# Performance work log

Hardware: AMD Instinct MI355X
Metric: run time of the kernel (lower is better)

The kernel has to match this reference:

```python
import jax, jax.numpy as jnp
import numpy as np

jax.config.update("jax_enable_x64", True)

N_QUBITS = 21
N_LAYERS = 2
N_PARAMS = (N_LAYERS + 1) * N_QUBITS  # 63

# CNOT in |ctrl,tgt> basis, reshaped to (c_out, t_out, c_in, t_in)
_CNOT = jnp.array([[1, 0, 0, 0],
                   [0, 1, 0, 0],
                   [0, 0, 0, 1],
                   [0, 0, 1, 0]], dtype=jnp.complex128).reshape(2, 2, 2, 2)


def _ry(theta):
    # RY(theta) = [[cos(t/2), -sin(t/2)], [sin(t/2), cos(t/2)]]
    c = jnp.cos(theta * 0.5).astype(jnp.complex128)
    s = jnp.sin(theta * 0.5).astype(jnp.complex128)
    return jnp.stack([jnp.stack([c, -s]), jnp.stack([s, c])])


def _apply_1q(state, gate, q):
    # Contract 2x2 gate into qubit axis q of the (2,)*n state tensor.
    state = jnp.tensordot(gate, state, axes=((1,), (q,)))
    return jnp.moveaxis(state, 0, q)


def _apply_cnot(state, q):
    # CNOT with control q, target q+1 (qubit 0 = most-significant axis).
    state = jnp.tensordot(_CNOT, state, axes=((2, 3), (q, q + 1)))
    return jnp.moveaxis(state, (0, 1), (q, q + 1))


def setup_inputs() -> dict:
    key = jax.random.key(0)
    params = jax.random.uniform(key, (N_PARAMS,), dtype=jnp.float32) * (2.0 * np.pi)
    return {"params": params}


def reference(params):
    p = params.astype(jnp.float64)
    # |0...0> as a (2,)*n tensor
    state = jnp.zeros((2,) * N_QUBITS, dtype=jnp.complex128)
    state = state.at[(0,) * N_QUBITS].set(1.0 + 0.0j)
    idx = 0
    for _ in range(N_LAYERS):
        for q in range(N_QUBITS):
            state = _apply_1q(state, _ry(p[idx]), q)
            idx += 1
        for q in range(N_QUBITS - 1):
            state = _apply_cnot(state, q)
    for q in range(N_QUBITS):
        state = _apply_1q(state, _ry(p[idx]), q)
        idx += 1
    state = state.reshape(-1)  # (2**N_QUBITS,)
    return state / jnp.linalg.norm(state)
```

## Files before the change

kernel.cpp:

```cpp
#include <hip/hip_runtime.h>


#define NQ 21
#define NSTATE (1 << NQ)
#define SW(t) ((t) + ((t) >> 5))

typedef float f32x4 __attribute__((ext_vector_type(4)));

__device__ __forceinline__ float sel(const float* cs, const float* sn, int i,
                                     int bit) {
  return bit ? sn[i] : cs[i];
}

template <int BIT, int N>
__device__ __forceinline__ void ry_bf(float (&v)[N], float c, float s) {
#pragma unroll
  for (int m = 0; m < N; ++m)
    if ((m & (1 << BIT)) == 0) {
      float a = v[m], b = v[m | (1 << BIT)];
      v[m] = c * a - s * b;
      v[m | (1 << BIT)] = s * a + c * b;
    }
}

template <int CBIT, int TBIT, int N>
__device__ __forceinline__ void cnot_rr(float (&v)[N]) {
#pragma unroll
  for (int m = 0; m < N; ++m)
    if ((m & (1 << CBIT)) && !(m & (1 << TBIT))) {
      float t = v[m];
      v[m] = v[m | (1 << TBIT)];
      v[m | (1 << TBIT)] = t;
    }
}

template <int TBIT, int N>
__device__ __forceinline__ void cswap_bf(float (&v)[N], bool cond) {
#pragma unroll
  for (int m = 0; m < N; ++m)
    if ((m & (1 << TBIT)) == 0) {
      float a = v[m], b = v[m | (1 << TBIT)];
      v[m] = cond ? b : a;
      v[m | (1 << TBIT)] = cond ? a : b;
    }
}

template <int MASK, int N>
__device__ __forceinline__ void ry_shfl(float (&u)[N], float c, float s,
                                        int lane) {
  const float ss = (lane & MASK) ? s : -s;
#pragma unroll
  for (int e = 0; e < N; ++e) {
    float w = __shfl_xor(u[e], MASK);
    u[e] = c * u[e] + ss * w;
  }
}

template <int CMASK, int TMASK, int N>
__device__ __forceinline__ void cnot_shfl(float (&u)[N], int lane) {
  const bool ctrl = (lane & CMASK) != 0;
#pragma unroll
  for (int e = 0; e < N; ++e) {
    float w = __shfl_xor(u[e], TMASK);
    u[e] = ctrl ? w : u[e];
  }
}

__global__ __launch_bounds__(512) void fused(const float* __restrict__ p,
                                             float* __restrict__ out,
                                             int outmode) {
  __shared__ float cs[63], sn[63];
  __shared__ float ex[8448];
  const int tid = threadIdx.x;
  const int bid = blockIdx.x;
  if (tid < 63) {
    float h = 0.5f * p[tid];
    cs[tid] = cosf(h);
    sn[tid] = sinf(h);
  }
  __syncthreads();

  const int lane = tid & 63;
  float u[16];
  {
    const int zh = (lane & 31) << 4;
    const int c = lane >> 5;
#pragma unroll
    for (int e = 0; e < 16; ++e) {
      const int z = zh | e;
      const int gz = z ^ (z >> 1);
      float F = sel(cs, sn, 0, (z >> 8) & 1);
#pragma unroll
      for (int j = 0; j < 8; ++j) F *= sel(cs, sn, 8 - j, (gz >> j) & 1);
      u[e] = ((z & 1) == c) ? F : 0.0f;
    }
  }
  ry_shfl<16>(u, cs[21], sn[21], lane);
  ry_shfl<8>(u, cs[22], sn[22], lane);
  ry_shfl<4>(u, cs[23], sn[23], lane);
  ry_shfl<2>(u, cs[24], sn[24], lane);
  ry_shfl<1>(u, cs[25], sn[25], lane);
  ry_bf<3>(u, cs[26], sn[26]);
  ry_bf<2>(u, cs[27], sn[27]);
  ry_bf<1>(u, cs[28], sn[28]);
  ry_bf<0>(u, cs[29], sn[29]);
  cnot_shfl<16, 8>(u, lane);
  cnot_shfl<8, 4>(u, lane);
  cnot_shfl<4, 2>(u, lane);
  cnot_shfl<2, 1>(u, lane);
  cswap_bf<3>(u, (lane & 1) != 0);
  cnot_rr<3, 2>(u);
  cnot_rr<2, 1>(u);
  cnot_rr<1, 0>(u);
  ry_shfl<16>(u, cs[42], sn[42], lane);
  ry_shfl<8>(u, cs[43], sn[43], lane);
  ry_shfl<4>(u, cs[44], sn[44], lane);
  ry_shfl<2>(u, cs[45], sn[45], lane);
  ry_shfl<1>(u, cs[46], sn[46], lane);
  ry_bf<3>(u, cs[47], sn[47]);
  ry_bf<2>(u, cs[48], sn[48]);
  ry_bf<1>(u, cs[49], sn[49]);

  const int b7 = bid & 7;
  float ue0 = u[0], ue1 = u[1];
#pragma unroll
  for (int k = 1; k < 8; ++k) {
    ue0 = (b7 == k) ? u[2 * k] : ue0;
    ue1 = (b7 == k) ? u[2 * k + 1] : ue1;
  }
  const int l0 = bid >> 3;
  const float a00 = __shfl(ue0, l0);
  const float a01 = __shfl(ue0, 32 | l0);
  const float a10 = __shfl(ue1, l0);
  const float a11 = __shfl(ue1, 32 | l0);
  float W[2][2];
  W[0][0] = a00 * cs[9] + a01 * sn[9];
  W[0][1] = a00 * sn[9] + a01 * cs[9];
  W[1][0] = a10 * cs[9] + a11 * sn[9];
  W[1][1] = a10 * sn[9] + a11 * cs[9];

  float v[16];
  {
    const int gt = tid ^ (tid >> 1);
    float tcommon = 1.0f;
#pragma unroll
    for (int b = 0; b < 8; ++b)
      tcommon *= sel(cs, sn, 20 - b, (gt >> b) & 1);
    const int t8 = (tid >> 8) & 1;
#pragma unroll
    for (int r = 0; r < 16; ++r) {
      const int gr = r ^ (r >> 1);
      float prod = tcommon * W[(r >> 3) & 1][(r >> 2) & 1];
      prod *= sel(cs, sn, 12, t8 ^ (r & 1));
      prod *= sel(cs, sn, 11, gr & 1);
      prod *= sel(cs, sn, 10, (gr >> 1) & 1);
      v[r] = prod;
    }
  }

  ry_bf<2>(v, cs[30], sn[30]);
  ry_bf<1>(v, cs[31], sn[31]);
  ry_bf<0>(v, cs[32], sn[32]);
  cnot_rr<3, 2>(v);
  cnot_rr<2, 1>(v);
  cnot_rr<1, 0>(v);
  ry_bf<3>(v, cs[50], sn[50]);
  ry_bf<2>(v, cs[51], sn[51]);
  ry_bf<1>(v, cs[52], sn[52]);

#pragma unroll
  for (int r = 0; r < 16; ++r) ex[SW((r << 9) | tid)] = v[r];
  __syncthreads();
#pragma unroll
  for (int r = 0; r < 16; ++r)
    v[r] = ex[SW(((tid >> 6) << 10) | (r << 6) | (tid & 63))];
  __syncthreads();

  ry_bf<2>(v, cs[33], sn[33]);
  ry_bf<1>(v, cs[34], sn[34]);
  ry_bf<0>(v, cs[35], sn[35]);
  cnot_rr<3, 2>(v);
  cnot_rr<2, 1>(v);
  cnot_rr<1, 0>(v);
  ry_bf<3>(v, cs[53], sn[53]);
  ry_bf<2>(v, cs[54], sn[54]);
  ry_bf<1>(v, cs[55], sn[55]);

#pragma unroll
  for (int r = 0; r < 16; ++r)
    ex[SW(((tid >> 6) << 10) | (r << 6) | (tid & 63))] = v[r];
  __syncthreads();
#pragma unroll
  for (int r = 0; r < 16; ++r)
    v[r] = ex[SW(((tid >> 3) << 7) | (r << 3) | (tid & 7))];
  __syncthreads();

  ry_bf<2>(v, cs[36], sn[36]);
  ry_bf<1>(v, cs[37], sn[37]);
  ry_bf<0>(v, cs[38], sn[38]);
  cnot_rr<3, 2>(v);
  cnot_rr<2, 1>(v);
  cnot_rr<1, 0>(v);
  ry_bf<3>(v, cs[56], sn[56]);
  ry_bf<2>(v, cs[57], sn[57]);
  ry_bf<1>(v, cs[58], sn[58]);

#pragma unroll
  for (int r = 0; r < 16; ++r)
    ex[SW(((tid >> 3) << 7) | (r << 3) | (tid & 7))] = v[r];
  __syncthreads();
#pragma unroll
  for (int r = 0; r < 16; ++r) v[r] = ex[SW((tid << 4) | r)];

  ry_bf<2>(v, cs[39], sn[39]);
  ry_bf<1>(v, cs[40], sn[40]);
  ry_bf<0>(v, cs[41], sn[41]);
  cnot_rr<3, 2>(v);
  cnot_rr<2, 1>(v);
  cnot_rr<1, 0>(v);
  ry_bf<3>(v, cs[59], sn[59]);
  ry_bf<2>(v, cs[60], sn[60]);
  ry_bf<1>(v, cs[61], sn[61]);
  ry_bf<0>(v, cs[62], sn[62]);

  const int base = (bid << 13) | (tid << 4);
  if (outmode == 2) {
    f32x4* o4 = (f32x4*)out;
#pragma unroll
    for (int i = 0; i < 8; ++i) {
      f32x4 w = {v[2 * i], 0.0f, v[2 * i + 1], 0.0f};
      __builtin_nontemporal_store(w, &o4[(base >> 1) + i]);
    }
  } else {
    f32x4* o4 = (f32x4*)(out + base);
#pragma unroll
    for (int j = 0; j < 4; ++j) {
      f32x4 w = {v[4 * j], v[4 * j + 1], v[4 * j + 2], v[4 * j + 3]};
      __builtin_nontemporal_store(w, &o4[j]);
    }
  }
}

extern "C" void kernel_launch(void* const* d_in, const int* in_sizes, int n_in,
                              void* d_out, int out_size, void* d_ws,
                              size_t ws_size, hipStream_t stream) {
  const float* p = (const float*)d_in[0];
  float* out = (float*)d_out;
  const int outmode = (out_size == 2 * NSTATE) ? 2 : 1;
  fused<<<256, 512, 0, stream>>>(p, out, outmode);
}
```

Baseline: 68.91 us.

## Replace wavefront shuffle prefix simulation with closed-form per-block transfer-matrix recurrence

The per-block 2x2 boundary coefficients W are now computed with a scalar recurrence over the first eight qubits, a transfer-matrix product selected by the block index bits. This replaces simulating a 1024-amplitude prefix state per wavefront with many cross-lane shuffles and then picking one entry. The change removes shuffle and ALU work at the start of every block and lowers register pressure. Launch bounds also gain a minimum of 4 blocks per CU to encourage higher occupancy. The risk is a mismatch in the algebraic derivation, such as bit ordering or sign conventions.

```diff
diff --git a/kernel.cpp b/kernel.cpp
--- a/kernel.cpp
+++ b/kernel.cpp
@@ -34,41 +34,9 @@
     }
 }
 
-template <int TBIT, int N>
-__device__ __forceinline__ void cswap_bf(float (&v)[N], bool cond) {
-#pragma unroll
-  for (int m = 0; m < N; ++m)
-    if ((m & (1 << TBIT)) == 0) {
-      float a = v[m], b = v[m | (1 << TBIT)];
-      v[m] = cond ? b : a;
-      v[m | (1 << TBIT)] = cond ? a : b;
-    }
-}
-
-template <int MASK, int N>
-__device__ __forceinline__ void ry_shfl(float (&u)[N], float c, float s,
-                                        int lane) {
-  const float ss = (lane & MASK) ? s : -s;
-#pragma unroll
-  for (int e = 0; e < N; ++e) {
-    float w = __shfl_xor(u[e], MASK);
-    u[e] = c * u[e] + ss * w;
-  }
-}
-
-template <int CMASK, int TMASK, int N>
-__device__ __forceinline__ void cnot_shfl(float (&u)[N], int lane) {
-  const bool ctrl = (lane & CMASK) != 0;
-#pragma unroll
-  for (int e = 0; e < N; ++e) {
-    float w = __shfl_xor(u[e], TMASK);
-    u[e] = ctrl ? w : u[e];
-  }
-}
-
-__global__ __launch_bounds__(512) void fused(const float* __restrict__ p,
-                                             float* __restrict__ out,
-                                             int outmode) {
+__global__ __launch_bounds__(512, 4) void fused(const float* __restrict__ p,
+                                                float* __restrict__ out,
+                                                int outmode) {
   __shared__ float cs[63], sn[63];
   __shared__ float ex[8448];
   const int tid = threadIdx.x;
@@ -80,64 +48,54 @@
   }
   __syncthreads();
 
-  const int lane = tid & 63;
-  float u[16];
+  float W[2][2];
   {
-    const int zh = (lane & 31) << 4;
-    const int c = lane >> 5;
-#pragma unroll
-    for (int e = 0; e < 16; ++e) {
-      const int z = zh | e;
-      const int gz = z ^ (z >> 1);
-      float F = sel(cs, sn, 0, (z >> 8) & 1);
-#pragma unroll
-      for (int j = 0; j < 8; ++j) F *= sel(cs, sn, 8 - j, (gz >> j) & 1);
-      u[e] = ((z & 1) == c) ? F : 0.0f;
-    }
-  }
-  ry_shfl<16>(u, cs[21], sn[21], lane);
-  ry_shfl<8>(u, cs[22], sn[22], lane);
-  ry_shfl<4>(u, cs[23], sn[23], lane);
-  ry_shfl<2>(u, cs[24], sn[24], lane);
-  ry_shfl<1>(u, cs[25], sn[25], lane);
-  ry_bf<3>(u, cs[26], sn[26]);
-  ry_bf<2>(u, cs[27], sn[27]);
-  ry_bf<1>(u, cs[28], sn[28]);
-  ry_bf<0>(u, cs[29], sn[29]);
-  cnot_shfl<16, 8>(u, lane);
-  cnot_shfl<8, 4>(u, lane);
-  cnot_shfl<4, 2>(u, lane);
-  cnot_shfl<2, 1>(u, lane);
-  cswap_bf<3>(u, (lane & 1) != 0);
-  cnot_rr<3, 2>(u);
-  cnot_rr<2, 1>(u);
-  cnot_rr<1, 0>(u);
-  ry_shfl<16>(u, cs[42], sn[42], lane);
-  ry_shfl<8>(u, cs[43], sn[43], lane);
-  ry_shfl<4>(u, cs[44], sn[44], lane);
-  ry_shfl<2>(u, cs[45], sn[45], lane);
-  ry_shfl<1>(u, cs[46], sn[46], lane);
-  ry_bf<3>(u, cs[47], sn[47]);
-  ry_bf<2>(u, cs[48], sn[48]);
-  ry_bf<1>(u, cs[49], sn[49]);
-
-  const int b7 = bid & 7;
-  float ue0 = u[0], ue1 = u[1];
-#pragma unroll
-  for (int k = 1; k < 8; ++k) {
-    ue0 = (b7 == k) ? u[2 * k] : ue0;
-    ue1 = (b7 == k) ? u[2 * k + 1] : ue1;
-  }
-  const int l0 = bid >> 3;
-  const float a00 = __shfl(ue0, l0);
-  const float a01 = __shfl(ue0, 32 | l0);
-  const float a10 = __shfl(ue1, l0);
-  const float a11 = __shfl(ue1, 32 | l0);
-  float W[2][2];
-  W[0][0] = a00 * cs[9] + a01 * sn[9];
-  W[0][1] = a00 * sn[9] + a01 * cs[9];
-  W[1][0] = a10 * cs[9] + a11 * sn[9];
-  W[1][1] = a10 * sn[9] + a11 * cs[9];
+    const int b0 = (bid >> 7) & 1;
+    const float c30 = cs[42], s30 = sn[42];
+    const float r00 = b0 ? s30 : c30;
+    const float r01 = b0 ? c30 : -s30;
+    const float c20 = cs[21], s20 = sn[21];
+    const float c10 = cs[0], s10 = sn[0];
+    float w00 = r00 * c20 * c10;
+    float w01 = r00 * (-s20) * s10;
+    float w10 = r01 * s20 * c10;
+    float w11 = r01 * c20 * s10;
+#pragma unroll
+    for (int q = 1; q <= 7; ++q) {
+      const int bq = (bid >> (7 - q)) & 1;
+      const float c1 = cs[q], s1 = sn[q];
+      const float c2 = cs[21 + q], s2 = sn[21 + q];
+      const float c3 = cs[42 + q], s3 = sn[42 + q];
+      const float h00 = c1 * w00 + s1 * w01;
+      const float h01 = c1 * w10 + s1 * w11;
+      const float h10 = s1 * w00 + c1 * w01;
+      const float h11 = s1 * w10 + c1 * w11;
+      const float m00 = c2 * h00 + s2 * h01;
+      const float m01 = s2 * h00 + c2 * h01;
+      const float m10 = -s2 * h10 + c2 * h11;
+      const float m11 = c2 * h10 - s2 * h11;
+      const float r0 = bq ? s3 : c3;
+      const float r1 = bq ? c3 : -s3;
+      w00 = r0 * m00;
+      w01 = r0 * m10;
+      w10 = r1 * m01;
+      w11 = r1 * m11;
+    }
+    const float c18 = cs[8], s18 = sn[8];
+    const float c28 = cs[29], s28 = sn[29];
+    const float hh00 = c18 * w00 + s18 * w01;
+    const float hh01 = c18 * w10 + s18 * w11;
+    const float hh10 = s18 * w00 + c18 * w01;
+    const float hh11 = s18 * w10 + c18 * w11;
+    const float a00 = c28 * hh00 + s28 * hh01;
+    const float a10 = s28 * hh00 + c28 * hh01;
+    const float a01 = -s28 * hh10 + c28 * hh11;
+    const float a11 = c28 * hh10 - s28 * hh11;
+    W[0][0] = a00 * cs[9] + a01 * sn[9];
+    W[0][1] = a00 * sn[9] + a01 * cs[9];
+    W[1][0] = a10 * cs[9] + a11 * sn[9];
+    W[1][1] = a10 * sn[9] + a11 * cs[9];
+  }
 
   float v[16];
   {
```

Result: faster. 62.58 us (-9.2%).
